# Optimization experiments

Hardware: AMD Instinct MI355X
Metric: run time of the kernel (lower is better)

Reference implementation:

```python
import jax, jax.numpy as jnp
import numpy as np

B, H, N, D = 1, 1, 4096, 1024
DFF = 4096
LN_EPS = 1e-5


def _layer_norm(x, g, b):
    m = jnp.mean(x, axis=-1, keepdims=True)
    v = jnp.mean(jnp.square(x - m), axis=-1, keepdims=True)
    return (x - m) * jax.lax.rsqrt(v + LN_EPS) * g + b


def _mha(q, k, v, W, b):
    # NOTE: source has no 1/sqrt(d) scaling -- kept faithful.
    a = jnp.einsum('bhnd,bhmd->bhnm', q, k)
    a = jax.nn.softmax(a, axis=-1)
    o = jnp.einsum('bhnm,bhmd->bhnd', a, v)
    bb, hh, nn, dd = o.shape
    o = o.transpose(0, 2, 1, 3).reshape(bb, nn, hh * dd)  # b n (h d)
    return o @ W.T + b


def setup_inputs() -> dict:
    key = jax.random.key(0)
    ks = jax.random.split(key, 16)
    s = 0.02
    return {
        'x': jax.random.normal(ks[0], (B, H, N, D), jnp.float32),
        'x_encoder': jax.random.normal(ks[1], (B, H, N, D), jnp.float32),
        'pos': jax.random.normal(ks[2], (B, H, N, D), jnp.float32),
        'query_pos': jax.random.normal(ks[3], (B, H, N, D), jnp.float32),
        'Wp_sa': jax.random.normal(ks[4], (D, D), jnp.float32) * s,
        'bp_sa': jnp.zeros((D,), jnp.float32),
        'Wp_ca': jax.random.normal(ks[5], (D, D), jnp.float32) * s,
        'bp_ca': jnp.zeros((D,), jnp.float32),
        'W1': jax.random.normal(ks[6], (DFF, D), jnp.float32) * s,
        'b1': jnp.zeros((DFF,), jnp.float32),
        'W2': jax.random.normal(ks[7], (D, DFF), jnp.float32) * s,
        'b2': jnp.zeros((D,), jnp.float32),
        'g_sa': jnp.ones((D,), jnp.float32),
        'be_sa': jnp.zeros((D,), jnp.float32),
        'g_ca': jnp.ones((D,), jnp.float32),
        'be_ca': jnp.zeros((D,), jnp.float32),
        'g_ff': jnp.ones((D,), jnp.float32),
        'be_ff': jnp.zeros((D,), jnp.float32),
    }


def reference(x, x_encoder, pos, query_pos, Wp_sa, bp_sa, Wp_ca, bp_ca,
              W1, b1, W2, b2, g_sa, be_sa, g_ca, be_ca, g_ff, be_ff):
    # self-attention block
    n1 = _layer_norm(x, g_sa, be_sa)
    qk = n1 + pos
    x = _mha(qk, qk, n1, Wp_sa, bp_sa) + x
    # cross-attention block
    n2 = _layer_norm(x, g_ca, be_ca)
    q = n2 + query_pos
    k = x_encoder + pos
    x = _mha(q, k, x_encoder, Wp_ca, bp_ca) + x
    # feed-forward block (exact GELU, matching torch nn.GELU default)
    n3 = _layer_norm(x, g_ff, be_ff)
    h = jax.nn.gelu(n3 @ W1.T + b1, approximate=False)
    x = (h @ W2.T + b2) + x
    return x
```

## Files before the change

### kernel.cpp

```cpp
#include <hip/hip_runtime.h>
#include <hip/hip_fp16.h>
#include <cstdint>
#include <cstdio>

#define NROW 4096
#define DMODEL 1024
#define DFF_ 4096

typedef _Float16 f16;
typedef _Float16 f16x4 __attribute__((ext_vector_type(4)));
typedef _Float16 f16x8 __attribute__((ext_vector_type(8)));
typedef float f32x4 __attribute__((ext_vector_type(4)));

__device__ __forceinline__ void g2l16(const void* g, void* l) {
  __builtin_amdgcn_global_load_lds((const __attribute__((address_space(1))) void*)g,
                                   (__attribute__((address_space(3))) void*)l,
                                   16, 0, 0);
}

__global__ __launch_bounds__(256) void cvt_f32_f16(const float* __restrict__ in,
                                                   f16* __restrict__ out, long n4) {
  for (long i = (long)blockIdx.x * blockDim.x + threadIdx.x; i < n4;
       i += (long)gridDim.x * blockDim.x) {
    float4 a = ((const float4*)in)[i];
    f16x4 h = {(f16)a.x, (f16)a.y, (f16)a.z, (f16)a.w};
    ((f16x4*)out)[i] = h;
  }
}

__global__ __launch_bounds__(256) void add_cvt(const float* __restrict__ xe,
                                               const float* __restrict__ pos,
                                               f16* __restrict__ k16,
                                               f16* __restrict__ xe16, long n4) {
  for (long i = (long)blockIdx.x * blockDim.x + threadIdx.x; i < n4;
       i += (long)gridDim.x * blockDim.x) {
    float4 a = ((const float4*)xe)[i];
    float4 p = ((const float4*)pos)[i];
    f16x4 k = {(f16)(a.x + p.x), (f16)(a.y + p.y), (f16)(a.z + p.z), (f16)(a.w + p.w)};
    f16x4 v = {(f16)a.x, (f16)a.y, (f16)a.z, (f16)a.w};
    ((f16x4*)k16)[i] = k;
    ((f16x4*)xe16)[i] = v;
  }
}

__global__ __launch_bounds__(256) void ln_row(const float* __restrict__ x,
                                              const float* __restrict__ g,
                                              const float* __restrict__ b,
                                              const float* __restrict__ pos,
                                              f16* __restrict__ nout,
                                              f16* __restrict__ qout) {
  const int row = blockIdx.x, tid = threadIdx.x;
  const float4 xv = ((const float4*)(x + (long)row * DMODEL))[tid];
  float s = xv.x + xv.y + xv.z + xv.w;
  float ss = xv.x * xv.x + xv.y * xv.y + xv.z * xv.z + xv.w * xv.w;
  for (int o = 32; o; o >>= 1) { s += __shfl_xor(s, o); ss += __shfl_xor(ss, o); }
  __shared__ float rs[4], rss[4];
  const int wid = tid >> 6, lane = tid & 63;
  if (!lane) { rs[wid] = s; rss[wid] = ss; }
  __syncthreads();
  s = rs[0] + rs[1] + rs[2] + rs[3];
  ss = rss[0] + rss[1] + rss[2] + rss[3];
  const float mean = s * (1.f / DMODEL);
  const float var = ss * (1.f / DMODEL) - mean * mean;
  const float rstd = rsqrtf(var + 1e-5f);
  const float4 gv = ((const float4*)g)[tid];
  const float4 bv = ((const float4*)b)[tid];
  float4 nv;
  nv.x = (xv.x - mean) * rstd * gv.x + bv.x;
  nv.y = (xv.y - mean) * rstd * gv.y + bv.y;
  nv.z = (xv.z - mean) * rstd * gv.z + bv.z;
  nv.w = (xv.w - mean) * rstd * gv.w + bv.w;
  if (nout) {
    f16x4 h = {(f16)nv.x, (f16)nv.y, (f16)nv.z, (f16)nv.w};
    *(f16x4*)&nout[(long)row * DMODEL + tid * 4] = h;
  }
  float4 pv = {0.f, 0.f, 0.f, 0.f};
  if (pos) pv = ((const float4*)(pos + (long)row * DMODEL))[tid];
  f16x4 q = {(f16)(nv.x + pv.x), (f16)(nv.y + pv.y), (f16)(nv.z + pv.z), (f16)(nv.w + pv.w)};
  *(f16x4*)&qout[(long)row * DMODEL + tid * 4] = q;
}

__global__ __launch_bounds__(256) void softmax_row(const float* __restrict__ S,
                                                   f16* __restrict__ P) {
  const int row = blockIdx.x, tid = threadIdx.x;
  const float4* Sr = (const float4*)(S + (long)row * NROW);
  float4 v[4];
  float m = -1e30f;
#pragma unroll
  for (int i = 0; i < 4; i++) {
    v[i] = Sr[tid + i * 256];
    m = fmaxf(m, fmaxf(fmaxf(v[i].x, v[i].y), fmaxf(v[i].z, v[i].w)));
  }
  for (int o = 32; o; o >>= 1) m = fmaxf(m, __shfl_xor(m, o));
  __shared__ float red[4], red2[4];
  const int wid = tid >> 6, lane = tid & 63;
  if (!lane) red[wid] = m;
  __syncthreads();
  m = fmaxf(fmaxf(red[0], red[1]), fmaxf(red[2], red[3]));
  float sum = 0.f;
#pragma unroll
  for (int i = 0; i < 4; i++) {
    v[i].x = __expf(v[i].x - m); v[i].y = __expf(v[i].y - m);
    v[i].z = __expf(v[i].z - m); v[i].w = __expf(v[i].w - m);
    sum += v[i].x + v[i].y + v[i].z + v[i].w;
  }
  for (int o = 32; o; o >>= 1) sum += __shfl_xor(sum, o);
  if (!lane) red2[wid] = sum;
  __syncthreads();
  sum = red2[0] + red2[1] + red2[2] + red2[3];
  const float r = 1.f / sum;
  f16* Pr = P + (long)row * NROW;
#pragma unroll
  for (int i = 0; i < 4; i++) {
    f16x4 h = {(f16)(v[i].x * r), (f16)(v[i].y * r), (f16)(v[i].z * r), (f16)(v[i].w * r)};
    *(f16x4*)&Pr[(tid + i * 256) * 4] = h;
  }
}

__global__ __launch_bounds__(256) void transpose_h(const f16* __restrict__ in,
                                                   f16* __restrict__ out, int R, int C) {
  __shared__ f16 t[64][72];
  const int tid = threadIdx.x;
  const int r0 = blockIdx.y * 64, c0 = blockIdx.x * 64;
  const int tr = tid >> 4, tc = (tid & 15) * 4;
#pragma unroll
  for (int rr = 0; rr < 4; rr++) {
    int row = rr * 16 + tr;
    f16x4 v = *(const f16x4*)&in[(long)(r0 + row) * C + c0 + tc];
    *(f16x4*)&t[row][tc] = v;
  }
  __syncthreads();
#pragma unroll
  for (int rr = 0; rr < 4; rr++) {
    int row = rr * 16 + tr;
    f16x4 o = {t[tc + 0][row], t[tc + 1][row], t[tc + 2][row], t[tc + 3][row]};
    *(f16x4*)&out[(long)(c0 + row) * R + r0 + tc] = o;
  }
}

enum { EPI_F32 = 0, EPI_F16 = 1, EPI_PROJ = 2, EPI_GELU = 3, EPI_FINAL = 4 };

template <int BN, int BK>
__device__ __forceinline__ void stage_tile(const f16* __restrict__ Arow,
                                           const f16* __restrict__ Brow, int K, int kt,
                                           int tid, f16* Asd, f16* Bsd) {
  constexpr int CH = BK / 8;
  const int k0 = kt * BK;
#pragma unroll
  for (int rr = 0; rr < 128 * CH / 256; ++rr) {
    int e = rr * 256 + tid;
    int row = e / CH, c = e % CH;
    int cs = c ^ (row & (CH - 1));
    g2l16(Arow + (long)row * K + k0 + cs * 8, Asd + e * 8);
  }
#pragma unroll
  for (int rr = 0; rr < BN * CH / 256; ++rr) {
    int e = rr * 256 + tid;
    int row = e / CH, c = e % CH;
    int cs = c ^ (row & (CH - 1));
    g2l16(Brow + (long)row * K + k0 + cs * 8, Bsd + e * 8);
  }
  __builtin_amdgcn_sched_barrier(0);
}

template <int NJ, int BK>
__device__ __forceinline__ void compute_tile(const f16* Asd, const f16* Bsd, int wm,
                                             int wn, int lr, int lk4,
                                             f32x4 (&acc)[4][NJ]) {
  constexpr int CH = BK / 8;
#pragma unroll
  for (int s = 0; s < BK / 32; ++s) {
    const int g = s * 4 + lk4;
    f16x8 av[4], bv[NJ];
#pragma unroll
    for (int i = 0; i < 4; i++) {
      int row = wm + i * 16 + lr;
      int slot = g ^ (row & (CH - 1));
      av[i] = *(const f16x8*)&Asd[row * BK + slot * 8];
    }
#pragma unroll
    for (int j = 0; j < NJ; j++) {
      int row = wn + j * 16 + lr;
      int slot = g ^ (row & (CH - 1));
      bv[j] = *(const f16x8*)&Bsd[row * BK + slot * 8];
    }
#pragma unroll
    for (int i = 0; i < 4; i++)
#pragma unroll
      for (int j = 0; j < NJ; j++)
        acc[i][j] = __builtin_amdgcn_mfma_f32_16x16x32_f16(av[i], bv[j], acc[i][j], 0, 0, 0);
  }
}

template <int EPI, int BN, int BK>
__global__ __launch_bounds__(256) void gemm_nt(const f16* __restrict__ A,
                                               const f16* __restrict__ B, int K,
                                               void* __restrict__ Cout, int ldc,
                                               const float* __restrict__ bias,
                                               const float* __restrict__ res) {
  constexpr int NJ = BN / 32;
  __shared__ f16 As0[128 * BK];
  __shared__ f16 As1[128 * BK];
  __shared__ f16 Bs0[BN * BK];
  __shared__ f16 Bs1[BN * BK];
  const int tid = threadIdx.x;
  const int wid = tid >> 6, lane = tid & 63;
  const int wm = (wid >> 1) * 64, wn = (wid & 1) * (BN / 2);
  const int lr = lane & 15, lk4 = lane >> 4;
  const long bm = (long)blockIdx.y * 128;
  const long bn = (long)blockIdx.x * BN;

  f32x4 zero = {0.f, 0.f, 0.f, 0.f};
  f32x4 acc[4][NJ];
#pragma unroll
  for (int i = 0; i < 4; i++)
#pragma unroll
    for (int j = 0; j < NJ; j++) acc[i][j] = zero;

  const f16* Arow = A + bm * K;
  const f16* Brow = B + bn * K;
  const int nkt = K / BK;

  stage_tile<BN, BK>(Arow, Brow, K, 0, tid, As0, Bs0);
  __syncthreads();

  int kt = 0;
  for (; kt + 2 < nkt; kt += 2) {
    stage_tile<BN, BK>(Arow, Brow, K, kt + 1, tid, As1, Bs1);
    compute_tile<NJ, BK>(As0, Bs0, wm, wn, lr, lk4, acc);
    __syncthreads();
    stage_tile<BN, BK>(Arow, Brow, K, kt + 2, tid, As0, Bs0);
    compute_tile<NJ, BK>(As1, Bs1, wm, wn, lr, lk4, acc);
    __syncthreads();
  }
  stage_tile<BN, BK>(Arow, Brow, K, nkt - 1, tid, As1, Bs1);
  compute_tile<NJ, BK>(As0, Bs0, wm, wn, lr, lk4, acc);
  __syncthreads();
  compute_tile<NJ, BK>(As1, Bs1, wm, wn, lr, lk4, acc);

  const int r0 = (int)bm + wm + (lane >> 4) * 4;
  const int c0 = (int)bn + wn + (lane & 15);
#pragma unroll
  for (int i = 0; i < 4; i++) {
#pragma unroll
    for (int j = 0; j < NJ; j++) {
      const int c = c0 + j * 16;
      float bcol = 0.f;
      if (EPI == EPI_PROJ || EPI == EPI_GELU || EPI == EPI_FINAL) bcol = bias[c];
#pragma unroll
      for (int q = 0; q < 4; q++) {
        const int r = r0 + i * 16 + q;
        const long idx = (long)r * ldc + c;
        const float v = acc[i][j][q];
        if (EPI == EPI_F32) {
          ((float*)Cout)[idx] = v;
        } else if (EPI == EPI_F16) {
          ((f16*)Cout)[idx] = (f16)v;
        } else if (EPI == EPI_PROJ || EPI == EPI_FINAL) {
          ((float*)Cout)[idx] = v + bcol + res[idx];
        } else {
          const float h = v + bcol;
          const float gg = 0.5f * h * (1.f + erff(h * 0.70710678118654752f));
          ((f16*)Cout)[idx] = (f16)gg;
        }
      }
    }
  }
}

extern "C" void kernel_launch(void* const* d_in, const int* in_sizes, int n_in,
                              void* d_out, int out_size, void* d_ws, size_t ws_size,
                              hipStream_t stream) {
  const float* x = (const float*)d_in[0];
  const float* x_encoder = (const float*)d_in[1];
  const float* pos = (const float*)d_in[2];
  const float* query_pos = (const float*)d_in[3];
  const float* Wp_sa = (const float*)d_in[4];
  const float* bp_sa = (const float*)d_in[5];
  const float* Wp_ca = (const float*)d_in[6];
  const float* bp_ca = (const float*)d_in[7];
  const float* W1 = (const float*)d_in[8];
  const float* b1 = (const float*)d_in[9];
  const float* W2 = (const float*)d_in[10];
  const float* b2 = (const float*)d_in[11];
  const float* g_sa = (const float*)d_in[12];
  const float* be_sa = (const float*)d_in[13];
  const float* g_ca = (const float*)d_in[14];
  const float* be_ca = (const float*)d_in[15];
  const float* g_ff = (const float*)d_in[16];
  const float* be_ff = (const float*)d_in[17];

  const size_t MB = 1024 * 1024;
  char* ws = (char*)d_ws;
  f16* wpsa16 = (f16*)(ws + 0 * MB);
  f16* wpca16 = (f16*)(ws + 2 * MB);
  f16* w116 = (f16*)(ws + 4 * MB);
  f16* w216 = (f16*)(ws + 12 * MB);
  f16* q16 = (f16*)(ws + 20 * MB);
  f16* k16 = (f16*)(ws + 28 * MB);
  f16* n16 = (f16*)(ws + 36 * MB);
  f16* vT = (f16*)(ws + 44 * MB);
  f16* o16 = (f16*)(ws + 52 * MB);
  float* x1 = (float*)(ws + 60 * MB);
  float* x2 = (float*)(ws + 76 * MB);
  float* scores = (float*)(ws + 92 * MB);
  f16* h16 = (f16*)(ws + 92 * MB);
  f16* P16 = (f16*)(ws + 156 * MB);

  if (ws_size < (size_t)188 * MB) {
    fprintf(stderr, "kernel_launch: ws too small (%zu bytes, need %zu)\n", ws_size,
            (size_t)188 * MB);
    return;
  }

  cvt_f32_f16<<<1024, 256, 0, stream>>>(Wp_sa, wpsa16, (long)DMODEL * DMODEL / 4);
  cvt_f32_f16<<<1024, 256, 0, stream>>>(Wp_ca, wpca16, (long)DMODEL * DMODEL / 4);
  cvt_f32_f16<<<2048, 256, 0, stream>>>(W1, w116, (long)DFF_ * DMODEL / 4);
  cvt_f32_f16<<<2048, 256, 0, stream>>>(W2, w216, (long)DMODEL * DFF_ / 4);

  ln_row<<<NROW, 256, 0, stream>>>(x, g_sa, be_sa, pos, n16, q16);
  transpose_h<<<dim3(DMODEL / 64, NROW / 64), 256, 0, stream>>>(n16, vT, NROW, DMODEL);
  gemm_nt<EPI_F32, 128, 32><<<dim3(32, 32), 256, 0, stream>>>(q16, q16, DMODEL, scores,
                                                              NROW, nullptr, nullptr);
  softmax_row<<<NROW, 256, 0, stream>>>(scores, P16);
  gemm_nt<EPI_F16, 64, 64><<<dim3(16, 32), 256, 0, stream>>>(P16, vT, NROW, o16, DMODEL,
                                                             nullptr, nullptr);
  gemm_nt<EPI_PROJ, 64, 64><<<dim3(16, 32), 256, 0, stream>>>(o16, wpsa16, DMODEL, x1,
                                                              DMODEL, bp_sa, x);

  ln_row<<<NROW, 256, 0, stream>>>(x1, g_ca, be_ca, query_pos, nullptr, q16);
  add_cvt<<<2048, 256, 0, stream>>>(x_encoder, pos, k16, n16, (long)NROW * DMODEL / 4);
  transpose_h<<<dim3(DMODEL / 64, NROW / 64), 256, 0, stream>>>(n16, vT, NROW, DMODEL);
  gemm_nt<EPI_F32, 128, 32><<<dim3(32, 32), 256, 0, stream>>>(q16, k16, DMODEL, scores,
                                                              NROW, nullptr, nullptr);
  softmax_row<<<NROW, 256, 0, stream>>>(scores, P16);
  gemm_nt<EPI_F16, 64, 64><<<dim3(16, 32), 256, 0, stream>>>(P16, vT, NROW, o16, DMODEL,
                                                             nullptr, nullptr);
  gemm_nt<EPI_PROJ, 64, 64><<<dim3(16, 32), 256, 0, stream>>>(o16, wpca16, DMODEL, x2,
                                                              DMODEL, bp_ca, x1);

  ln_row<<<NROW, 256, 0, stream>>>(x2, g_ff, be_ff, nullptr, nullptr, q16);
  gemm_nt<EPI_GELU, 128, 32><<<dim3(32, 32), 256, 0, stream>>>(q16, w116, DMODEL, h16,
                                                               DFF_, b1, nullptr);
  gemm_nt<EPI_FINAL, 64, 64><<<dim3(16, 32), 256, 0, stream>>>(h16, w216, DFF_,
                                                               (float*)d_out, DMODEL, b2,
                                                               x2);
}
```

Baseline: 425.5 us.

## Add 256x256 ping-pong pipelined GEMM for score and FFN1 products

Adds a new 512-thread GEMM kernel with 256x256 output tiles, split into four 128x128 quadrants. It keeps four LDS buffers so global-to-LDS loads run ahead of the MFMA phases, using explicit vmcnt waits, barriers and priority raises. It replaces the 128x128 gemm_nt for the two attention score GEMMs and the FFN1 GELU GEMM, with the aim of more operand reuse and better overlap of memory traffic with compute. The cost is heavy LDS use (128 KB) and many accumulator registers, which limits occupancy. The grid of 256 blocks may also underfill the 256 CUs' scheduling slack, and the hand-written wait counts could be fragile.

```diff
diff --git a/kernel.cpp b/kernel.cpp
--- a/kernel.cpp
+++ b/kernel.cpp
@@ -139,6 +139,132 @@
 }
 
 enum { EPI_F32 = 0, EPI_F16 = 1, EPI_PROJ = 2, EPI_GELU = 3, EPI_FINAL = 4 };
+
+#define VM4 asm volatile("s_waitcnt vmcnt(4)" ::: "memory")
+#define VM0 asm volatile("s_waitcnt vmcnt(0)" ::: "memory")
+#define NOP (void)0
+
+#define PH(MQ, NQ, ASP, BSP, STG, WAITC)                                           \
+  {                                                                                \
+    f16x8 av[4][2], bv[2][2];                                                      \
+    _Pragma("unroll") for (int m = 0; m < 4; ++m)                                  \
+      _Pragma("unroll") for (int kk = 0; kk < 2; ++kk) {                           \
+        const int r_ = wr * 64 + m * 16 + lr;                                      \
+        av[m][kk] = *(const f16x8*)&(ASP)[r_ * 64 + (((kk * 4 + lk4) ^ (lr & 7)) << 3)]; \
+      }                                                                            \
+    _Pragma("unroll") for (int n = 0; n < 2; ++n)                                  \
+      _Pragma("unroll") for (int kk = 0; kk < 2; ++kk) {                           \
+        const int r_ = wc * 32 + n * 16 + lr;                                      \
+        bv[n][kk] = *(const f16x8*)&(BSP)[r_ * 64 + (((kk * 4 + lk4) ^ (lr & 7)) << 3)]; \
+      }                                                                            \
+    STG;                                                                           \
+    __builtin_amdgcn_sched_barrier(0);                                             \
+    WAITC;                                                                         \
+    __builtin_amdgcn_s_barrier();                                                  \
+    __builtin_amdgcn_s_setprio(1);                                                 \
+    _Pragma("unroll") for (int m = 0; m < 4; ++m)                                  \
+      _Pragma("unroll") for (int n = 0; n < 2; ++n)                                \
+        _Pragma("unroll") for (int kk = 0; kk < 2; ++kk)                           \
+          acc[MQ][NQ][m][n] = __builtin_amdgcn_mfma_f32_16x16x32_f16(              \
+              av[m][kk], bv[n][kk], acc[MQ][NQ][m][n], 0, 0, 0);                   \
+    __builtin_amdgcn_s_setprio(0);                                                 \
+    __builtin_amdgcn_sched_barrier(0);                                             \
+    __builtin_amdgcn_s_barrier();                                                  \
+    __builtin_amdgcn_sched_barrier(0);                                             \
+  }
+
+template <int EPI>
+__global__ __launch_bounds__(512) void gemm256(const f16* __restrict__ A,
+                                               const f16* __restrict__ B, int K,
+                                               void* __restrict__ Cout, int ldc,
+                                               const float* __restrict__ bias) {
+  __shared__ f16 As[4][128 * 64];
+  __shared__ f16 Bs[4][128 * 64];
+  const int tid = threadIdx.x;
+  const int wid = tid >> 6, lane = tid & 63;
+  const int wr = wid >> 2, wc = wid & 3;
+  const int lr = lane & 15, lk4 = lane >> 4;
+  const long bm = (long)blockIdx.y * 256, bn = (long)blockIdx.x * 256;
+  const f16* Abase = A + bm * K;
+  const f16* Bbase = B + bn * K;
+  const int nkt = K >> 6;
+
+  auto stage = [&](const f16* rowBase, int k0, f16* dst) {
+#pragma unroll
+    for (int r2 = 0; r2 < 2; ++r2) {
+      int e = r2 * 512 + tid;
+      int row = e >> 3, c = e & 7;
+      g2l16(rowBase + (long)row * K + k0 + ((c ^ (row & 7)) << 3), dst + e * 8);
+    }
+  };
+
+  f32x4 acc[2][2][4][2];
+#pragma unroll
+  for (int a = 0; a < 2; ++a)
+#pragma unroll
+    for (int b = 0; b < 2; ++b)
+#pragma unroll
+      for (int m = 0; m < 4; ++m)
+#pragma unroll
+        for (int n = 0; n < 2; ++n) acc[a][b][m][n] = f32x4{0.f, 0.f, 0.f, 0.f};
+
+  stage(Abase, 0, As[0]);
+  stage(Bbase, 0, Bs[0]);
+  stage(Bbase + (long)128 * K, 0, Bs[1]);
+  stage(Abase + (long)128 * K, 0, As[1]);
+  stage(Abase, 64, As[2]);
+  stage(Bbase, 64, Bs[2]);
+  __builtin_amdgcn_sched_barrier(0);
+  VM4;
+  __builtin_amdgcn_s_barrier();
+  __builtin_amdgcn_sched_barrier(0);
+
+  int t = 0;
+  for (; t <= nkt - 4; t += 2) {
+    PH(0, 0, As[0], Bs[0], stage(Bbase + (long)128 * K, (t + 1) * 64, Bs[3]), NOP)
+    PH(0, 1, As[0], Bs[1], stage(Abase + (long)128 * K, (t + 1) * 64, As[3]), NOP)
+    PH(1, 0, As[1], Bs[0], stage(Abase, (t + 2) * 64, As[0]), NOP)
+    PH(1, 1, As[1], Bs[1], stage(Bbase, (t + 2) * 64, Bs[0]), VM4)
+    PH(0, 0, As[2], Bs[2], stage(Bbase + (long)128 * K, (t + 2) * 64, Bs[1]), NOP)
+    PH(0, 1, As[2], Bs[3], stage(Abase + (long)128 * K, (t + 2) * 64, As[1]), NOP)
+    PH(1, 0, As[3], Bs[2], stage(Abase, (t + 3) * 64, As[2]), NOP)
+    PH(1, 1, As[3], Bs[3], stage(Bbase, (t + 3) * 64, Bs[2]), VM4)
+  }
+  PH(0, 0, As[0], Bs[0], stage(Bbase + (long)128 * K, (nkt - 1) * 64, Bs[3]), NOP)
+  PH(0, 1, As[0], Bs[1], stage(Abase + (long)128 * K, (nkt - 1) * 64, As[3]), NOP)
+  PH(1, 0, As[1], Bs[0], NOP, NOP)
+  PH(1, 1, As[1], Bs[1], NOP, VM0)
+  PH(0, 0, As[2], Bs[2], NOP, NOP)
+  PH(0, 1, As[2], Bs[3], NOP, NOP)
+  PH(1, 0, As[3], Bs[2], NOP, NOP)
+  PH(1, 1, As[3], Bs[3], NOP, NOP)
+
+  const int l4 = lane >> 4, lf = lane & 15;
+#pragma unroll
+  for (int mq = 0; mq < 2; ++mq)
+#pragma unroll
+    for (int nq = 0; nq < 2; ++nq)
+#pragma unroll
+      for (int m = 0; m < 4; ++m)
+#pragma unroll
+        for (int n = 0; n < 2; ++n) {
+          const long r = bm + mq * 128 + wr * 64 + m * 16 + l4 * 4;
+          const long cc = bn + nq * 128 + wc * 32 + n * 16 + lf;
+          float bcol = 0.f;
+          if (EPI == EPI_GELU) bcol = bias[cc];
+#pragma unroll
+          for (int q = 0; q < 4; ++q) {
+            const long idx = (r + q) * ldc + cc;
+            const float v = acc[mq][nq][m][n][q];
+            if (EPI == EPI_F32) {
+              ((float*)Cout)[idx] = v;
+            } else {
+              const float h = v + bcol;
+              ((f16*)Cout)[idx] = (f16)(0.5f * h * (1.f + erff(h * 0.70710678118654752f)));
+            }
+          }
+        }
+}
 
 template <int BN, int BK>
 __device__ __forceinline__ void stage_tile(const f16* __restrict__ Arow,
@@ -320,8 +446,8 @@
 
   ln_row<<<NROW, 256, 0, stream>>>(x, g_sa, be_sa, pos, n16, q16);
   transpose_h<<<dim3(DMODEL / 64, NROW / 64), 256, 0, stream>>>(n16, vT, NROW, DMODEL);
-  gemm_nt<EPI_F32, 128, 32><<<dim3(32, 32), 256, 0, stream>>>(q16, q16, DMODEL, scores,
-                                                              NROW, nullptr, nullptr);
+  gemm256<EPI_F32><<<dim3(16, 16), 512, 0, stream>>>(q16, q16, DMODEL, scores, NROW,
+                                                     nullptr);
   softmax_row<<<NROW, 256, 0, stream>>>(scores, P16);
   gemm_nt<EPI_F16, 64, 64><<<dim3(16, 32), 256, 0, stream>>>(P16, vT, NROW, o16, DMODEL,
                                                              nullptr, nullptr);
@@ -331,8 +457,8 @@
   ln_row<<<NROW, 256, 0, stream>>>(x1, g_ca, be_ca, query_pos, nullptr, q16);
   add_cvt<<<2048, 256, 0, stream>>>(x_encoder, pos, k16, n16, (long)NROW * DMODEL / 4);
   transpose_h<<<dim3(DMODEL / 64, NROW / 64), 256, 0, stream>>>(n16, vT, NROW, DMODEL);
-  gemm_nt<EPI_F32, 128, 32><<<dim3(32, 32), 256, 0, stream>>>(q16, k16, DMODEL, scores,
-                                                              NROW, nullptr, nullptr);
+  gemm256<EPI_F32><<<dim3(16, 16), 512, 0, stream>>>(q16, k16, DMODEL, scores, NROW,
+                                                     nullptr);
   softmax_row<<<NROW, 256, 0, stream>>>(scores, P16);
   gemm_nt<EPI_F16, 64, 64><<<dim3(16, 32), 256, 0, stream>>>(P16, vT, NROW, o16, DMODEL,
                                                              nullptr, nullptr);
@@ -340,8 +466,7 @@
                                                               DMODEL, bp_ca, x1);
 
   ln_row<<<NROW, 256, 0, stream>>>(x2, g_ff, be_ff, nullptr, nullptr, q16);
-  gemm_nt<EPI_GELU, 128, 32><<<dim3(32, 32), 256, 0, stream>>>(q16, w116, DMODEL, h16,
-                                                               DFF_, b1, nullptr);
+  gemm256<EPI_GELU><<<dim3(16, 16), 512, 0, stream>>>(q16, w116, DMODEL, h16, DFF_, b1);
   gemm_nt<EPI_FINAL, 64, 64><<<dim3(16, 32), 256, 0, stream>>>(h16, w216, DFF_,
                                                                (float*)d_out, DMODEL, b2,
                                                                x2);
```

Measured after the change: 416.7 us. 2.1% less time.
